# Performance work log

Hardware: AMD Instinct MI355X
Metric: run time of the kernel (lower is better)

The kernel has to match this reference:

```python
import jax, jax.numpy as jnp
import numpy as np
import math

N_SRC = 100000
N_DST0 = 30000
N_DST1 = 8000
E0 = 200000
E1 = 80000
H, D = 4, 64


def gat_conv(h_src, h_dst, src, dst, W, al, ar, b, n_dst):
    """DGL GATConv (allow_zero_in_degree=True): shared fc, LeakyReLU(0.2), edge softmax."""
    z_src = (h_src @ W).reshape(-1, H, D)              # [Ns,H,D]
    z_dst = (h_dst @ W).reshape(-1, H, D)              # [Nd,H,D]
    el = jnp.sum(z_src * al, axis=-1)                  # [Ns,H]
    er = jnp.sum(z_dst * ar, axis=-1)                  # [Nd,H]
    e = jax.nn.leaky_relu(el[src] + er[dst], 0.2)      # [E,H]
    emax = jax.ops.segment_max(e, dst, num_segments=n_dst)
    emax = jnp.where(jnp.isfinite(emax), emax, 0.0)
    ex = jnp.exp(e - emax[dst])
    denom = jax.ops.segment_sum(ex, dst, num_segments=n_dst)
    denom = jnp.where(denom > 0, denom, 1.0)
    alpha = ex / denom[dst]                            # [E,H]
    out = jax.ops.segment_sum(alpha[:, :, None] * z_src[src], dst, num_segments=n_dst)
    return out + b.reshape(1, H, D)                    # [Nd,H,D]


def attn_pool(feat):
    """Self attention over relation/head slots, then mean over slots (attention(f,f,f).mean(dim=1))."""
    d = feat.shape[-1]
    scores = jnp.einsum('nsd,ntd->nst', feat, feat) / math.sqrt(d)
    p = jax.nn.softmax(scores, axis=-1)
    out = jnp.einsum('nst,ntd->nsd', p, feat)
    return out.mean(axis=1)                            # [N,d]


def rgat_layer(xu, xi, eii, eiu, eui, W, al, ar, b, n_dst_u, n_dst_i):
    du, di = xu[:n_dst_u], xi[:n_dst_i]
    # sorted canonical etypes: ('item','ii','item') < ('item','iu','user') < ('user','ui','item')
    out_ii = gat_conv(xi, di, eii[0], eii[1], W[0], al[0], ar[0], b[0], n_dst_i)
    out_iu = gat_conv(xi, du, eiu[0], eiu[1], W[1], al[1], ar[1], b[1], n_dst_u)
    out_ui = gat_conv(xu, di, eui[0], eui[1], W[2], al[2], ar[2], b[2], n_dst_i)
    feat_u = out_iu                                    # [Nu, H, D]
    feat_i = jnp.concatenate([out_ii, out_ui], axis=1) # [Ni, 2H, D]
    hu = attn_pool(feat_u)
    hi = attn_pool(feat_i)
    return jnp.concatenate([du, hu], axis=1), jnp.concatenate([di, hi], axis=1)


def setup_inputs() -> dict:
    key = jax.random.key(0)
    ks = jax.random.split(key, 24)
    inp = {
        'x_user': jax.random.normal(ks[0], (N_SRC, 64), jnp.float32),
        'x_item': jax.random.normal(ks[1], (N_SRC, 64), jnp.float32),
        'e0_ii_src': jax.random.randint(ks[2], (E0,), 0, N_SRC, jnp.int32),
        'e0_ii_dst': jax.random.randint(ks[3], (E0,), 0, N_DST0, jnp.int32),
        'e0_iu_src': jax.random.randint(ks[4], (E0,), 0, N_SRC, jnp.int32),
        'e0_iu_dst': jax.random.randint(ks[5], (E0,), 0, N_DST0, jnp.int32),
        'e0_ui_src': jax.random.randint(ks[6], (E0,), 0, N_SRC, jnp.int32),
        'e0_ui_dst': jax.random.randint(ks[7], (E0,), 0, N_DST0, jnp.int32),
        'e1_ii_src': jax.random.randint(ks[8], (E1,), 0, N_DST0, jnp.int32),
        'e1_ii_dst': jax.random.randint(ks[9], (E1,), 0, N_DST1, jnp.int32),
        'e1_iu_src': jax.random.randint(ks[10], (E1,), 0, N_DST0, jnp.int32),
        'e1_iu_dst': jax.random.randint(ks[11], (E1,), 0, N_DST1, jnp.int32),
        'e1_ui_src': jax.random.randint(ks[12], (E1,), 0, N_DST0, jnp.int32),
        'e1_ui_dst': jax.random.randint(ks[13], (E1,), 0, N_DST1, jnp.int32),
        'W0': jax.random.normal(ks[14], (3, 64, H * D), jnp.float32) * 0.1,
        'al0': jax.random.normal(ks[15], (3, H, D), jnp.float32) * 0.1,
        'ar0': jax.random.normal(ks[16], (3, H, D), jnp.float32) * 0.1,
        'b0': jnp.zeros((3, H * D), jnp.float32),
        'W1': jax.random.normal(ks[17], (3, 128, H * D), jnp.float32) * 0.1,
        'al1': jax.random.normal(ks[18], (3, H, D), jnp.float32) * 0.1,
        'ar1': jax.random.normal(ks[19], (3, H, D), jnp.float32) * 0.1,
        'b1': jnp.zeros((3, H * D), jnp.float32),
    }
    return inp


def reference(x_user, x_item,
              e0_ii_src, e0_ii_dst, e0_iu_src, e0_iu_dst, e0_ui_src, e0_ui_dst,
              e1_ii_src, e1_ii_dst, e1_iu_src, e1_iu_dst, e1_ui_src, e1_ui_dst,
              W0, al0, ar0, b0, W1, al1, ar1, b1):
    xu, xi = rgat_layer(x_user, x_item,
                        (e0_ii_src, e0_ii_dst), (e0_iu_src, e0_iu_dst), (e0_ui_src, e0_ui_dst),
                        W0, al0, ar0, b0, N_DST0, N_DST0)
    xu, xi = rgat_layer(xu, xi,
                        (e1_ii_src, e1_ii_dst), (e1_iu_src, e1_iu_dst), (e1_ui_src, e1_ui_dst),
                        W1, al1, ar1, b1, N_DST1, N_DST1)
    return jnp.concatenate([xu, xi], axis=0)  # [2*N_DST1, 128+64]
```

## Files before the change

kernel.cpp:

```cpp
#include <hip/hip_runtime.h>

#define NSRC   100000
#define NDST0  30000
#define NDST1  8000
#define E0N    200000
#define E1N    80000
#define HD     256
#define DD     64
#define CAPB   32

typedef short bf16x8 __attribute__((ext_vector_type(8)));
typedef float f32x4  __attribute__((ext_vector_type(4)));

static __device__ __forceinline__ unsigned short f2bf(float f) {
    unsigned u = __float_as_uint(f);
    u += 0x7fffu + ((u >> 16) & 1u);
    return (unsigned short)(u >> 16);
}
static __device__ __forceinline__ unsigned pack2(float a, float b) {
    return (unsigned)f2bf(a) | ((unsigned)f2bf(b) << 16);
}
static __device__ __forceinline__ void fma4(float4& a, float s, const float4& b) {
    a.x = fmaf(s, b.x, a.x); a.y = fmaf(s, b.y, a.y);
    a.z = fmaf(s, b.z, a.z); a.w = fmaf(s, b.w, a.w);
}
static __device__ __forceinline__ float dot4(const float4& a, const float4& b) {
    return fmaf(a.x, b.x, fmaf(a.y, b.y, fmaf(a.z, b.z, a.w * b.w)));
}
static __device__ __forceinline__ float4 ld_bf4(const unsigned short* p) {
    uint2 u = *reinterpret_cast<const uint2*>(p);
    float4 r;
    r.x = __uint_as_float(u.x << 16);
    r.y = __uint_as_float(u.x & 0xffff0000u);
    r.z = __uint_as_float(u.y << 16);
    r.w = __uint_as_float(u.y & 0xffff0000u);
    return r;
}

static __device__ void wlr_prep(const float* __restrict__ W, const float* __restrict__ al,
                                const float* __restrict__ ar, float* __restrict__ wl,
                                float* __restrict__ wr, int K, int tid)
{
    int r = tid / (K * 4);
    int rem = tid - r * K * 4;
    int k = rem >> 2, h = rem & 3;
    const float* wrow = W + (size_t)r * K * HD + (size_t)k * HD + h * DD;
    const float* a_l = al + r * HD + h * DD;
    const float* a_r = ar + r * HD + h * DD;
    float sl = 0.f, sr = 0.f;
    for (int d = 0; d < DD; ++d) {
        float w = wrow[d];
        sl = fmaf(w, a_l[d], sl);
        sr = fmaf(w, a_r[d], sr);
    }
    wl[r * 512 + k * 4 + h] = sl;
    wr[r * 512 + k * 4 + h] = sr;
}
static __device__ void wt_prep(const float* __restrict__ W, unsigned short* __restrict__ Wt,
                               int K, int r, int c)
{
    const float* Wr = W + (size_t)r * K * HD;
    unsigned short* Wtr = Wt + (size_t)r * 256 * K;
    for (int k = 0; k < K; k += 2) {
        float a = Wr[(size_t)k * HD + c];
        float b = Wr[(size_t)(k + 1) * HD + c];
        *reinterpret_cast<unsigned*>(Wtr + (size_t)c * K + k) = pack2(a, b);
    }
}
static __device__ void fill_soa(const int* __restrict__ ed, const int* __restrict__ es,
                                int* __restrict__ cnt, int* __restrict__ bsrc,
                                int E, int nd, int r, int e)
{
    if (e >= E) return;
    int d = ed[e];
    int c = atomicAdd(&cnt[(size_t)r * nd + d], 1);
    if (c < CAPB) bsrc[((size_t)c * 3 + r) * nd + d] = es[e];
}
template<int K>
static __device__ void prep_row(bool item, int row, int nd,
                                const float* __restrict__ XA, const float* __restrict__ XB,
                                const float* __restrict__ wl3, const float* __restrict__ wr3,
                                float* __restrict__ el3, float* __restrict__ er3)
{
    const float* X = item ? XA : XB;
    const float4* xv = reinterpret_cast<const float4*>(X + (size_t)row * K);
    const float4* wlAv = reinterpret_cast<const float4*>(item ? wl3 : wl3 + 1024);
    const float4* wlBv = reinterpret_cast<const float4*>(wl3 + 512);
    float4 aA = make_float4(0.f, 0.f, 0.f, 0.f), aB = aA;
    #pragma unroll
    for (int c = 0; c < K / 4; ++c) {
        float4 x4 = xv[c];
        fma4(aA, x4.x, wlAv[c * 4 + 0]); fma4(aA, x4.y, wlAv[c * 4 + 1]);
        fma4(aA, x4.z, wlAv[c * 4 + 2]); fma4(aA, x4.w, wlAv[c * 4 + 3]);
        if (item) {
            fma4(aB, x4.x, wlBv[c * 4 + 0]); fma4(aB, x4.y, wlBv[c * 4 + 1]);
            fma4(aB, x4.z, wlBv[c * 4 + 2]); fma4(aB, x4.w, wlBv[c * 4 + 3]);
        }
    }
    if (item) {
        *reinterpret_cast<float4*>(el3 + (size_t)row * 4) = aA;
        *reinterpret_cast<float4*>(el3 + (size_t)NSRC * 4 + (size_t)row * 4) = aB;
    } else {
        *reinterpret_cast<float4*>(el3 + (size_t)2 * NSRC * 4 + (size_t)row * 4) = aA;
    }
    if (row < nd) {
        const float4* wrAv = reinterpret_cast<const float4*>(item ? wr3 : wr3 + 512);
        const float4* wrBv = reinterpret_cast<const float4*>(wr3 + 1024);
        float4 rA = make_float4(0.f, 0.f, 0.f, 0.f), rB = rA;
        #pragma unroll
        for (int c = 0; c < K / 4; ++c) {
            float4 x4 = xv[c];
            fma4(rA, x4.x, wrAv[c * 4 + 0]); fma4(rA, x4.y, wrAv[c * 4 + 1]);
            fma4(rA, x4.z, wrAv[c * 4 + 2]); fma4(rA, x4.w, wrAv[c * 4 + 3]);
            if (item) {
                fma4(rB, x4.x, wrBv[c * 4 + 0]); fma4(rB, x4.y, wrBv[c * 4 + 1]);
                fma4(rB, x4.z, wrBv[c * 4 + 2]); fma4(rB, x4.w, wrBv[c * 4 + 3]);
            }
        }
        if (item) {
            *reinterpret_cast<float4*>(er3 + (size_t)row * 4) = rA;
            *reinterpret_cast<float4*>(er3 + (size_t)2 * NDST0 * 4 + (size_t)row * 4) = rB;
        } else {
            *reinterpret_cast<float4*>(er3 + (size_t)NDST0 * 4 + (size_t)row * 4) = rA;
        }
    }
}

__global__ void k_wsetup(const float* W0, const float* al0, const float* ar0,
                         const float* W1, const float* al1, const float* ar1,
                         float* wlA, float* wrA, unsigned short* WtA,
                         float* wlB, float* wrB, unsigned short* WtB)
{
    int bx = blockIdx.x, t = threadIdx.x;
    if (bx < 3)       wlr_prep(W0, al0, ar0, wlA, wrA, 64,  bx * 256 + t);
    else if (bx < 9)  wlr_prep(W1, al1, ar1, wlB, wrB, 128, (bx - 3) * 256 + t);
    else if (bx < 12) wt_prep(W0, WtA, 64,  bx - 9,  t);
    else              wt_prep(W1, WtB, 128, bx - 12, t);
}

__global__ __launch_bounds__(256) void k_fillprep(
    const int* ed0, const int* ed1, const int* ed2,
    const int* es0, const int* es1, const int* es2,
    const int* ed3, const int* ed4, const int* ed5,
    const int* es3, const int* es4, const int* es5,
    int* cntA, int* bsrcA, int* cntB, int* bsrcB,
    const float* x_item, const float* x_user,
    const float* wlA, const float* wrA,
    float* el3, float* er3,
    int bpr0, int bpr1, int bprP)
{
    int bx = blockIdx.x;
    int t = threadIdx.x;
    if (bx < 3 * bpr0) {
        int r = (bx >= 2 * bpr0) ? 2 : (bx >= bpr0 ? 1 : 0);
        int e = (bx - r * bpr0) * 256 + t;
        const int* ed = (r == 0) ? ed0 : (r == 1 ? ed1 : ed2);
        const int* es = (r == 0) ? es0 : (r == 1 ? es1 : es2);
        fill_soa(ed, es, cntA, bsrcA, E0N, NDST0, r, e);
        return;
    }
    bx -= 3 * bpr0;
    if (bx < 3 * bpr1) {
        int r = (bx >= 2 * bpr1) ? 2 : (bx >= bpr1 ? 1 : 0);
        int e = (bx - r * bpr1) * 256 + t;
        const int* ed = (r == 0) ? ed3 : (r == 1 ? ed4 : ed5);
        const int* es = (r == 0) ? es3 : (r == 1 ? es4 : es5);
        fill_soa(ed, es, cntB, bsrcB, E1N, NDST1, r, e);
        return;
    }
    bx -= 3 * bpr1;
    const bool item = bx < bprP;
    int row = (item ? bx : bx - bprP) * 256 + t;
    if (row >= NSRC) return;
    prep_row<64>(item, row, NDST0, x_item, x_user, wlA, wrA, el3, er3);
}

template<int K>
__global__ __launch_bounds__(256) void k_prep_x2(const float* __restrict__ XA,
                                                 const float* __restrict__ XB,
                                                 int M, int nd, int bpr,
                                                 const float* __restrict__ wl3,
                                                 const float* __restrict__ wr3,
                                                 float* __restrict__ el3,
                                                 float* __restrict__ er3)
{
    int bx = blockIdx.x;
    const bool item = bx < bpr;
    int row = (item ? bx : bx - bpr) * 256 + threadIdx.x;
    if (row >= M) return;
    prep_row<K>(item, row, nd, XA, XB, wl3, wr3, el3, er3);
}

template<int K>
__global__ __launch_bounds__(256) void k_agg3(const int* __restrict__ cnt,
                                              const int* __restrict__ bsrc,
                                              const float* __restrict__ el3,
                                              const float* __restrict__ er3,
                                              const float* __restrict__ xsA,
                                              const float* __restrict__ xsB,
                                              unsigned short* __restrict__ aggX,
                                              int nd, int bpr)
{
    constexpr int NV = K / 64;
    __shared__ float exs[256][4];
    int bx = blockIdx.x;
    int r = (bx >= 2 * bpr) ? 2 : (bx >= bpr ? 1 : 0);
    int wid = ((bx - r * bpr) * 256 + (int)threadIdx.x) >> 6;
    int lane = threadIdx.x & 63;
    if (wid >= nd) return;
    int q = lane & 15, g = lane >> 4;
    const float* el = el3 + (size_t)r * NSRC * 4;
    const float* xsrc = (r < 2) ? xsA : xsB;
    int c = cnt[(size_t)r * nd + wid]; if (c > CAPB) c = CAPB;
    float4 er4 = *reinterpret_cast<const float4*>(er3 + (size_t)r * NDST0 * 4 + (size_t)wid * 4);

    int s_own = 0;
    float4 ex_own = make_float4(0.f, 0.f, 0.f, 0.f);
    if (lane < c) {
        s_own = bsrc[((size_t)lane * 3 + r) * nd + wid];
        float4 e4 = *reinterpret_cast<const float4*>(el + (size_t)s_own * 4);
        e4.x += er4.x; e4.y += er4.y; e4.z += er4.z; e4.w += er4.w;
        e4.x = e4.x > 0.f ? e4.x : 0.2f * e4.x;
        e4.y = e4.y > 0.f ? e4.y : 0.2f * e4.y;
        e4.z = e4.z > 0.f ? e4.z : 0.2f * e4.z;
        e4.w = e4.w > 0.f ? e4.w : 0.2f * e4.w;
        ex_own.x = __expf(e4.x); ex_own.y = __expf(e4.y);
        ex_own.z = __expf(e4.z); ex_own.w = __expf(e4.w);
    }
    *reinterpret_cast<float4*>(&exs[threadIdx.x][0]) = ex_own;
    const int wavebase = threadIdx.x & 192;

    float4 acc[NV];
    #pragma unroll
    for (int v = 0; v < NV; ++v) acc[v] = make_float4(0.f, 0.f, 0.f, 0.f);
    float den = 0.f;

    for (int t = 0; t < c; ++t) {
        int s = __shfl(s_own, t, 64);
        float ex = exs[wavebase + t][g];
        const float4* xp = reinterpret_cast<const float4*>(xsrc + (size_t)s * K) + q * NV;
        #pragma unroll
        for (int v = 0; v < NV; ++v) fma4(acc[v], ex, xp[v]);
        den += ex;
    }
    float inv = den > 0.f ? 1.f / den : 0.f;
    unsigned short* op = aggX + (((size_t)r * nd + wid) * 4 + g) * K + q * 4 * NV;
    if (NV == 1) {
        uint2 w;
        w.x = pack2(acc[0].x * inv, acc[0].y * inv);
        w.y = pack2(acc[0].z * inv, acc[0].w * inv);
        *reinterpret_cast<uint2*>(op) = w;
    } else {
        uint4 w;
        w.x = pack2(acc[0].x * inv, acc[0].y * inv);
        w.y = pack2(acc[0].z * inv, acc[0].w * inv);
        w.z = pack2(acc[1].x * inv, acc[1].y * inv);
        w.w = pack2(acc[1].z * inv, acc[1].w * inv);
        *reinterpret_cast<uint4*>(op) = w;
    }
}

template<int K>
__global__ __launch_bounds__(256) void k_gemm3(const unsigned short* __restrict__ aggX,
                                               const unsigned short* __restrict__ Wt3,
                                               unsigned short* __restrict__ outb,
                                               int nd, int bpr)
{
    int bx = blockIdx.x;
    int r = (bx >= 2 * bpr) ? 2 : (bx >= bpr ? 1 : 0);
    const unsigned short* A  = aggX + (size_t)r * nd * 4 * K;
    const unsigned short* Wt = Wt3 + (size_t)r * 256 * K;
    unsigned short* ob = outb + (size_t)r * NDST0 * HD;
    const int lane = threadIdx.x & 63;
    const int wv = threadIdx.x >> 6;
    const int r0 = (bx - r * bpr) * 16;
    const int rr = lane & 15, kg = lane >> 4;
    f32x4 acc[4] = {{0.f,0.f,0.f,0.f},{0.f,0.f,0.f,0.f},{0.f,0.f,0.f,0.f},{0.f,0.f,0.f,0.f}};
    const unsigned short* ap = A + ((size_t)(r0 + rr) * 4 + wv) * K + kg * 8;
    #pragma unroll
    for (int kb = 0; kb < K; kb += 32) {
        bf16x8 a = *reinterpret_cast<const bf16x8*>(ap + kb);
        #pragma unroll
        for (int n = 0; n < 4; ++n) {
            const unsigned short* wp = Wt + (size_t)(wv * 64 + n * 16 + rr) * K + kb + kg * 8;
            bf16x8 b = *reinterpret_cast<const bf16x8*>(wp);
            acc[n] = __builtin_amdgcn_mfma_f32_16x16x32_bf16(a, b, acc[n], 0, 0, 0);
        }
    }
    #pragma unroll
    for (int n = 0; n < 4; ++n)
        #pragma unroll
        for (int i = 0; i < 4; ++i)
            ob[(size_t)(r0 + kg * 4 + i) * HD + wv * 64 + n * 16 + rr] = f2bf(acc[n][i]);
}

template<int S>
__global__ __launch_bounds__(256) void k_pool2(const unsigned short* __restrict__ srcA, const float* __restrict__ bA,
                                               const unsigned short* __restrict__ srcB, const float* __restrict__ bB,
                                               const float* __restrict__ base, int baseCols,
                                               float* __restrict__ dst, int pitch, int colOff, int n)
{
    int wid = (blockIdx.x * 256 + threadIdx.x) >> 6;
    int lane = threadIdx.x & 63;
    int node = wid * 4 + (lane >> 4);
    int q = lane & 15;
    if (node >= n) return;

    float4 f[S];
    #pragma unroll
    for (int s = 0; s < S; ++s) {
        const unsigned short* sp = (s < 4) ? (srcA + (size_t)node * HD + s * DD)
                                           : (srcB + (size_t)node * HD + (s - 4) * DD);
        const float* bp = (s < 4) ? (bA + s * DD) : (bB + (s - 4) * DD);
        float4 v = ld_bf4(sp + q * 4);
        float4 b = *reinterpret_cast<const float4*>(bp + q * 4);
        v.x += b.x; v.y += b.y; v.z += b.z; v.w += b.w;
        f[s] = v;
    }
    constexpr int NE = S * (S + 1) / 2;
    float gt[NE];
    {
        int idx = 0;
        #pragma unroll
        for (int s = 0; s < S; ++s)
            #pragma unroll
            for (int t = s; t < S; ++t)
                gt[idx++] = dot4(f[s], f[t]);
    }
    #pragma unroll
    for (int m = 1; m < 16; m <<= 1) {
        #pragma unroll
        for (int i = 0; i < NE; ++i) gt[i] += __shfl_xor(gt[i], m, 16);
    }
    auto Gv = [&](int s, int t) -> float {
        int a = s < t ? s : t, b2 = s < t ? t : s;
        return gt[a * S - a * (a - 1) / 2 + (b2 - a)];
    };
    float g[S];
    #pragma unroll
    for (int t = 0; t < S; ++t) g[t] = 0.f;
    #pragma unroll
    for (int s = 0; s < S; ++s) {
        float sc[S];
        float m = -1e30f;
        #pragma unroll
        for (int t = 0; t < S; ++t) { sc[t] = Gv(s, t) * 0.125f; m = sc[t] > m ? sc[t] : m; }
        float pe[S];
        float sum = 0.f;
        #pragma unroll
        for (int t = 0; t < S; ++t) { pe[t] = __expf(sc[t] - m); sum += pe[t]; }
        float inv = 1.f / sum;
        #pragma unroll
        for (int t = 0; t < S; ++t) g[t] += pe[t] * inv;
    }
    float4 o = make_float4(0.f, 0.f, 0.f, 0.f);
    #pragma unroll
    for (int t = 0; t < S; ++t) fma4(o, g[t], f[t]);
    const float is = 1.f / S;
    o.x *= is; o.y *= is; o.z *= is; o.w *= is;
    *reinterpret_cast<float4*>(dst + (size_t)node * pitch + colOff + q * 4) = o;
    for (int c = q * 4; c < baseCols; c += 64) {
        float4 v = *reinterpret_cast<const float4*>(base + (size_t)node * baseCols + c);
        *reinterpret_cast<float4*>(dst + (size_t)node * pitch + c) = v;
    }
}

extern "C" void kernel_launch(void* const* d_in, const int* in_sizes, int n_in,
                              void* d_out, int out_size, void* d_ws, size_t ws_size,
                              hipStream_t stream)
{
    const float* x_user = (const float*)d_in[0];
    const float* x_item = (const float*)d_in[1];
    const int* e_s[6] = { (const int*)d_in[2], (const int*)d_in[4], (const int*)d_in[6],
                          (const int*)d_in[8], (const int*)d_in[10], (const int*)d_in[12] };
    const int* e_d[6] = { (const int*)d_in[3], (const int*)d_in[5], (const int*)d_in[7],
                          (const int*)d_in[9], (const int*)d_in[11], (const int*)d_in[13] };
    const float* W0  = (const float*)d_in[14];
    const float* al0 = (const float*)d_in[15];
    const float* ar0 = (const float*)d_in[16];
    const float* b0  = (const float*)d_in[17];
    const float* W1  = (const float*)d_in[18];
    const float* al1 = (const float*)d_in[19];
    const float* ar1 = (const float*)d_in[20];
    const float* b1  = (const float*)d_in[21];
    float* out = (float*)d_out;
    (void)in_sizes; (void)n_in; (void)out_size; (void)ws_size;

    char* p = (char*)d_ws;
    auto take = [&](size_t bytes) { char* r = p; p += (bytes + 255) & ~(size_t)255; return r; };
    unsigned short* out3 = (unsigned short*)take((size_t)3 * NDST0 * HD * 2);
    float* xu1  = (float*)take((size_t)NDST0 * 128 * 4);
    float* xi1  = (float*)take((size_t)NDST0 * 128 * 4);
    unsigned short* aggX = (unsigned short*)take((size_t)3 * NDST0 * 4 * DD * 2);
    float* el3  = (float*)take((size_t)3 * NSRC * 4 * 4);
    float* er3  = (float*)take((size_t)3 * NDST0 * 4 * 4);
    int*   cntA = (int*)take((size_t)3 * NDST0 * 4);
    int*   cntB = (int*)take((size_t)3 * NDST1 * 4);
    int*   bsrcA = (int*)take((size_t)CAPB * 3 * NDST0 * 4);
    int*   bsrcB = (int*)take((size_t)CAPB * 3 * NDST1 * 4);
    unsigned short* WtA = (unsigned short*)take((size_t)3 * 256 * 64 * 2);
    unsigned short* WtB = (unsigned short*)take((size_t)3 * 256 * 128 * 2);
    float* wlA = (float*)take((size_t)3 * 512 * 4);
    float* wrA = (float*)take((size_t)3 * 512 * 4);
    float* wlB = (float*)take((size_t)3 * 512 * 4);
    float* wrB = (float*)take((size_t)3 * 512 * 4);

    unsigned short* out_ii = out3;
    unsigned short* out_iu = out3 + (size_t)NDST0 * HD;
    unsigned short* out_ui = out3 + (size_t)2 * NDST0 * HD;

    {
        size_t cntSpan = (size_t)((char*)cntB - (char*)cntA) + (size_t)3 * NDST1 * 4;
        hipMemsetAsync(cntA, 0, cntSpan, stream);
    }
    k_wsetup<<<15, 256, 0, stream>>>(W0, al0, ar0, W1, al1, ar1,
                                     wlA, wrA, WtA, wlB, wrB, WtB);
    const int bpr0 = (E0N + 255) / 256;
    const int bpr1 = (E1N + 255) / 256;
    const int bprP = (NSRC + 255) / 256;
    k_fillprep<<<3 * bpr0 + 3 * bpr1 + 2 * bprP, 256, 0, stream>>>(
        e_d[0], e_d[1], e_d[2], e_s[0], e_s[1], e_s[2],
        e_d[3], e_d[4], e_d[5], e_s[3], e_s[4], e_s[5],
        cntA, bsrcA, cntB, bsrcB,
        x_item, x_user, wlA, wrA, el3, er3,
        bpr0, bpr1, bprP);

    {
        const int bprA = (NDST0 + 3) / 4;
        k_agg3<64><<<3 * bprA, 256, 0, stream>>>(cntA, bsrcA, el3, er3, x_item, x_user,
                                                 aggX, NDST0, bprA);
        const int bprG = NDST0 / 16;
        k_gemm3<64><<<3 * bprG, 256, 0, stream>>>(aggX, WtA, out3, NDST0, bprG);
    }
    k_pool2<4><<<NDST0 / 16, 256, 0, stream>>>(out_iu, b0 + 256, out_iu, b0 + 256,
                                               x_user, 64, xu1, 128, 64, NDST0);
    k_pool2<8><<<NDST0 / 16, 256, 0, stream>>>(out_ii, b0, out_ui, b0 + 512,
                                               x_item, 64, xi1, 128, 64, NDST0);

    {
        const int bpr = (NDST0 + 255) / 256;
        k_prep_x2<128><<<2 * bpr, 256, 0, stream>>>(xi1, xu1, NDST0, NDST1, bpr,
                                                    wlB, wrB, el3, er3);
        const int bprA = (NDST1 + 3) / 4;
        k_agg3<128><<<3 * bprA, 256, 0, stream>>>(cntB, bsrcB, el3, er3, xi1, xu1,
                                                  aggX, NDST1, bprA);
        const int bprG = NDST1 / 16;
        k_gemm3<128><<<3 * bprG, 256, 0, stream>>>(aggX, WtB, out3, NDST1, bprG);
    }
    k_pool2<4><<<NDST1 / 16, 256, 0, stream>>>(out_iu, b1 + 256, out_iu, b1 + 256,
                                               xu1, 128, out, 192, 128, NDST1);
    k_pool2<8><<<NDST1 / 16, 256, 0, stream>>>(out_ii, b1, out_ui, b1 + 512,
                                               xi1, 128, out + (size_t)NDST1 * 192, 192, 128, NDST1);
}
```

Before: 320.6 us.

## Store per-destination edge buckets contiguously and pack src/exp pairs in shared memory

Changes the bucketed source list from a slot-major layout to a per-destination contiguous layout, so each wave reads its list with one coalesced load. The aggregation loop now reads source index and exp weight together from shared memory instead of doing a cross-lane shuffle plus a separate LDS read, and it is unrolled by two. The weight-setup kernel is merged into the edge-fill kernel, while the layer-0 el/er projection moves back into its own k_prep_x2 launch. The cost is a different launch structure and scattered atomic-slot writes into the contiguous buckets.

```diff
diff --git a/kernel.cpp b/kernel.cpp
--- a/kernel.cpp
+++ b/kernel.cpp
@@ -67,14 +67,14 @@
         *reinterpret_cast<unsigned*>(Wtr + (size_t)c * K + k) = pack2(a, b);
     }
 }
-static __device__ void fill_soa(const int* __restrict__ ed, const int* __restrict__ es,
+static __device__ void fill_aos(const int* __restrict__ ed, const int* __restrict__ es,
                                 int* __restrict__ cnt, int* __restrict__ bsrc,
                                 int E, int nd, int r, int e)
 {
     if (e >= E) return;
     int d = ed[e];
     int c = atomicAdd(&cnt[(size_t)r * nd + d], 1);
-    if (c < CAPB) bsrc[((size_t)c * 3 + r) * nd + d] = es[e];
+    if (c < CAPB) bsrc[((size_t)r * nd + d) * CAPB + c] = es[e];
 }
 template<int K>
 static __device__ void prep_row(bool item, int row, int nd,
@@ -126,28 +126,17 @@
     }
 }
 
-__global__ void k_wsetup(const float* W0, const float* al0, const float* ar0,
-                         const float* W1, const float* al1, const float* ar1,
-                         float* wlA, float* wrA, unsigned short* WtA,
-                         float* wlB, float* wrB, unsigned short* WtB)
-{
-    int bx = blockIdx.x, t = threadIdx.x;
-    if (bx < 3)       wlr_prep(W0, al0, ar0, wlA, wrA, 64,  bx * 256 + t);
-    else if (bx < 9)  wlr_prep(W1, al1, ar1, wlB, wrB, 128, (bx - 3) * 256 + t);
-    else if (bx < 12) wt_prep(W0, WtA, 64,  bx - 9,  t);
-    else              wt_prep(W1, WtB, 128, bx - 12, t);
-}
-
-__global__ __launch_bounds__(256) void k_fillprep(
+__global__ __launch_bounds__(256) void k_setup(
     const int* ed0, const int* ed1, const int* ed2,
     const int* es0, const int* es1, const int* es2,
     const int* ed3, const int* ed4, const int* ed5,
     const int* es3, const int* es4, const int* es5,
     int* cntA, int* bsrcA, int* cntB, int* bsrcB,
-    const float* x_item, const float* x_user,
-    const float* wlA, const float* wrA,
-    float* el3, float* er3,
-    int bpr0, int bpr1, int bprP)
+    const float* W0, const float* al0, const float* ar0,
+    const float* W1, const float* al1, const float* ar1,
+    float* wlA, float* wrA, unsigned short* WtA,
+    float* wlB, float* wrB, unsigned short* WtB,
+    int bpr0, int bpr1)
 {
     int bx = blockIdx.x;
     int t = threadIdx.x;
@@ -156,7 +145,7 @@
         int e = (bx - r * bpr0) * 256 + t;
         const int* ed = (r == 0) ? ed0 : (r == 1 ? ed1 : ed2);
         const int* es = (r == 0) ? es0 : (r == 1 ? es1 : es2);
-        fill_soa(ed, es, cntA, bsrcA, E0N, NDST0, r, e);
+        fill_aos(ed, es, cntA, bsrcA, E0N, NDST0, r, e);
         return;
     }
     bx -= 3 * bpr0;
@@ -165,14 +154,14 @@
         int e = (bx - r * bpr1) * 256 + t;
         const int* ed = (r == 0) ? ed3 : (r == 1 ? ed4 : ed5);
         const int* es = (r == 0) ? es3 : (r == 1 ? es4 : es5);
-        fill_soa(ed, es, cntB, bsrcB, E1N, NDST1, r, e);
+        fill_aos(ed, es, cntB, bsrcB, E1N, NDST1, r, e);
         return;
     }
     bx -= 3 * bpr1;
-    const bool item = bx < bprP;
-    int row = (item ? bx : bx - bprP) * 256 + t;
-    if (row >= NSRC) return;
-    prep_row<64>(item, row, NDST0, x_item, x_user, wlA, wrA, el3, er3);
+    if (bx < 3)       wlr_prep(W0, al0, ar0, wlA, wrA, 64,  bx * 256 + t);
+    else if (bx < 9)  wlr_prep(W1, al1, ar1, wlB, wrB, 128, (bx - 3) * 256 + t);
+    else if (bx < 12) wt_prep(W0, WtA, 64,  bx - 9,  t);
+    else              wt_prep(W1, WtB, 128, bx - 12, t);
 }
 
 template<int K>
@@ -202,43 +191,46 @@
                                               int nd, int bpr)
 {
     constexpr int NV = K / 64;
-    __shared__ float exs[256][4];
+    __shared__ float exs[4][64][8];
     int bx = blockIdx.x;
     int r = (bx >= 2 * bpr) ? 2 : (bx >= bpr ? 1 : 0);
     int wid = ((bx - r * bpr) * 256 + (int)threadIdx.x) >> 6;
     int lane = threadIdx.x & 63;
     if (wid >= nd) return;
-    int q = lane & 15, g = lane >> 4;
+    int q = lane & 15, g = lane >> 4, w = threadIdx.x >> 6;
     const float* el = el3 + (size_t)r * NSRC * 4;
     const float* xsrc = (r < 2) ? xsA : xsB;
     int c = cnt[(size_t)r * nd + wid]; if (c > CAPB) c = CAPB;
+    const int* lst = bsrc + ((size_t)r * nd + wid) * CAPB;
     float4 er4 = *reinterpret_cast<const float4*>(er3 + (size_t)r * NDST0 * 4 + (size_t)wid * 4);
 
-    int s_own = 0;
-    float4 ex_own = make_float4(0.f, 0.f, 0.f, 0.f);
     if (lane < c) {
-        s_own = bsrc[((size_t)lane * 3 + r) * nd + wid];
-        float4 e4 = *reinterpret_cast<const float4*>(el + (size_t)s_own * 4);
+        int s = lst[lane];
+        float4 e4 = *reinterpret_cast<const float4*>(el + (size_t)s * 4);
         e4.x += er4.x; e4.y += er4.y; e4.z += er4.z; e4.w += er4.w;
         e4.x = e4.x > 0.f ? e4.x : 0.2f * e4.x;
         e4.y = e4.y > 0.f ? e4.y : 0.2f * e4.y;
         e4.z = e4.z > 0.f ? e4.z : 0.2f * e4.z;
         e4.w = e4.w > 0.f ? e4.w : 0.2f * e4.w;
-        ex_own.x = __expf(e4.x); ex_own.y = __expf(e4.y);
-        ex_own.z = __expf(e4.z); ex_own.w = __expf(e4.w);
-    }
-    *reinterpret_cast<float4*>(&exs[threadIdx.x][0]) = ex_own;
-    const int wavebase = threadIdx.x & 192;
+        float sF = __int_as_float(s);
+        float4 h0 = make_float4(sF, __expf(e4.x), sF, __expf(e4.y));
+        float4 h1 = make_float4(sF, __expf(e4.z), sF, __expf(e4.w));
+        *reinterpret_cast<float4*>(&exs[w][lane][0]) = h0;
+        *reinterpret_cast<float4*>(&exs[w][lane][4]) = h1;
+    }
 
     float4 acc[NV];
     #pragma unroll
     for (int v = 0; v < NV; ++v) acc[v] = make_float4(0.f, 0.f, 0.f, 0.f);
     float den = 0.f;
-
+    const char* xb = reinterpret_cast<const char*>(xsrc) + q * (NV * 16);
+
+    #pragma unroll 2
     for (int t = 0; t < c; ++t) {
-        int s = __shfl(s_own, t, 64);
-        float ex = exs[wavebase + t][g];
-        const float4* xp = reinterpret_cast<const float4*>(xsrc + (size_t)s * K) + q * NV;
+        float2 se = *reinterpret_cast<const float2*>(&exs[w][t][g * 2]);
+        int s = __float_as_int(se.x);
+        float ex = se.y;
+        const float4* xp = reinterpret_cast<const float4*>(xb + (size_t)((unsigned)s * (K * 4)));
         #pragma unroll
         for (int v = 0; v < NV; ++v) fma4(acc[v], ex, xp[v]);
         den += ex;
@@ -246,17 +238,17 @@
     float inv = den > 0.f ? 1.f / den : 0.f;
     unsigned short* op = aggX + (((size_t)r * nd + wid) * 4 + g) * K + q * 4 * NV;
     if (NV == 1) {
-        uint2 w;
-        w.x = pack2(acc[0].x * inv, acc[0].y * inv);
-        w.y = pack2(acc[0].z * inv, acc[0].w * inv);
-        *reinterpret_cast<uint2*>(op) = w;
+        uint2 wv;
+        wv.x = pack2(acc[0].x * inv, acc[0].y * inv);
+        wv.y = pack2(acc[0].z * inv, acc[0].w * inv);
+        *reinterpret_cast<uint2*>(op) = wv;
     } else {
-        uint4 w;
-        w.x = pack2(acc[0].x * inv, acc[0].y * inv);
-        w.y = pack2(acc[0].z * inv, acc[0].w * inv);
-        w.z = pack2(acc[1].x * inv, acc[1].y * inv);
-        w.w = pack2(acc[1].z * inv, acc[1].w * inv);
-        *reinterpret_cast<uint4*>(op) = w;
+        uint4 wv;
+        wv.x = pack2(acc[0].x * inv, acc[0].y * inv);
+        wv.y = pack2(acc[0].z * inv, acc[0].w * inv);
+        wv.z = pack2(acc[1].x * inv, acc[1].y * inv);
+        wv.w = pack2(acc[1].z * inv, acc[1].w * inv);
+        *reinterpret_cast<uint4*>(op) = wv;
     }
 }
 
@@ -396,8 +388,8 @@
     float* er3  = (float*)take((size_t)3 * NDST0 * 4 * 4);
     int*   cntA = (int*)take((size_t)3 * NDST0 * 4);
     int*   cntB = (int*)take((size_t)3 * NDST1 * 4);
-    int*   bsrcA = (int*)take((size_t)CAPB * 3 * NDST0 * 4);
-    int*   bsrcB = (int*)take((size_t)CAPB * 3 * NDST1 * 4);
+    int*   bsrcA = (int*)take((size_t)3 * NDST0 * CAPB * 4);
+    int*   bsrcB = (int*)take((size_t)3 * NDST1 * CAPB * 4);
     unsigned short* WtA = (unsigned short*)take((size_t)3 * 256 * 64 * 2);
     unsigned short* WtB = (unsigned short*)take((size_t)3 * 256 * 128 * 2);
     float* wlA = (float*)take((size_t)3 * 512 * 4);
@@ -413,19 +405,19 @@
         size_t cntSpan = (size_t)((char*)cntB - (char*)cntA) + (size_t)3 * NDST1 * 4;
         hipMemsetAsync(cntA, 0, cntSpan, stream);
     }
-    k_wsetup<<<15, 256, 0, stream>>>(W0, al0, ar0, W1, al1, ar1,
-                                     wlA, wrA, WtA, wlB, wrB, WtB);
     const int bpr0 = (E0N + 255) / 256;
     const int bpr1 = (E1N + 255) / 256;
-    const int bprP = (NSRC + 255) / 256;
-    k_fillprep<<<3 * bpr0 + 3 * bpr1 + 2 * bprP, 256, 0, stream>>>(
+    k_setup<<<3 * bpr0 + 3 * bpr1 + 15, 256, 0, stream>>>(
         e_d[0], e_d[1], e_d[2], e_s[0], e_s[1], e_s[2],
         e_d[3], e_d[4], e_d[5], e_s[3], e_s[4], e_s[5],
         cntA, bsrcA, cntB, bsrcB,
-        x_item, x_user, wlA, wrA, el3, er3,
-        bpr0, bpr1, bprP);
+        W0, al0, ar0, W1, al1, ar1,
+        wlA, wrA, WtA, wlB, wrB, WtB, bpr0, bpr1);
 
     {
+        const int bprP = (NSRC + 255) / 256;
+        k_prep_x2<64><<<2 * bprP, 256, 0, stream>>>(x_item, x_user, NSRC, NDST0, bprP,
+                                                    wlA, wrA, el3, er3);
         const int bprA = (NDST0 + 3) / 4;
         k_agg3<64><<<3 * bprA, 256, 0, stream>>>(cntA, bsrcA, el3, er3, x_item, x_user,
                                                  aggX, NDST0, bprA);
@@ -438,9 +430,9 @@
                                                x_item, 64, xi1, 128, 64, NDST0);
 
     {
-        const int bpr = (NDST0 + 255) / 256;
-        k_prep_x2<128><<<2 * bpr, 256, 0, stream>>>(xi1, xu1, NDST0, NDST1, bpr,
-                                                    wlB, wrB, el3, er3);
+        const int bprP = (NDST0 + 255) / 256;
+        k_prep_x2<128><<<2 * bprP, 256, 0, stream>>>(xi1, xu1, NDST0, NDST1, bprP,
+                                                     wlB, wrB, el3, er3);
         const int bprA = (NDST1 + 3) / 4;
         k_agg3<128><<<3 * bprA, 256, 0, stream>>>(cntB, bsrcB, el3, er3, xi1, xu1,
                                                   aggX, NDST1, bprA);
```

Result: faster. 308.5 us (-3.8%).
